# Kernel tuning notes

Measured on AMD Instinct MI355X. Metric: run time of the kernel, lower is better.

## Reference

```python
import jax, jax.numpy as jnp
import numpy as np

DIM = 512
D_STATE = 16
D_CONV = 4
EXPAND = 2
D_INNER = EXPAND * DIM  # 1024
BATCH = 4
SEQLEN = 4096


def silu(v):
    return v * jax.nn.sigmoid(v)


def setup_inputs() -> dict:
    key = jax.random.key(0)
    ks = jax.random.split(key, 8)
    s = 0.02  # small init scale for stability
    return {
        "x": jax.random.normal(ks[0], (BATCH, SEQLEN, DIM), jnp.float32),
        "W_in": jax.random.normal(ks[1], (2 * D_INNER, DIM), jnp.float32) * s,
        "conv_w": jax.random.normal(ks[2], (D_INNER, 1, D_CONV), jnp.float32) * s,
        "conv_b": jax.random.normal(ks[3], (D_INNER,), jnp.float32) * s,
        "W_x": jax.random.normal(ks[4], (2 * D_STATE, D_INNER), jnp.float32) * s,
        "W_dt": jax.random.normal(ks[5], (D_STATE, D_INNER), jnp.float32) * s,
        "b_dt": jax.random.normal(ks[6], (D_STATE,), jnp.float32) * s,
        "A_log": jnp.log(jnp.arange(1, D_STATE + 1, dtype=jnp.float32))[None, :],
        "D_param": jnp.ones((D_INNER,), jnp.float32),
        "W_out": jax.random.normal(ks[7], (DIM, D_INNER), jnp.float32) * s,
    }


def reference(x, W_in, conv_w, conv_b, W_x, W_dt, b_dt, A_log, D_param, W_out):
    B, L, _ = x.shape
    # in_proj and split into x / res streams
    x_and_res = jnp.einsum('bld,ed->ble', x, W_in)          # [B,L,2*d_inner]
    xi, res = x_and_res[..., :D_INNER], x_and_res[..., D_INNER:]
    # causal depthwise conv1d (torch pads both sides by d_conv-1 then slices [:L]
    # == left-pad d_conv-1, no right pad)
    xc = jax.lax.conv_general_dilated(
        xi.transpose(0, 2, 1), conv_w, (1,), [(D_CONV - 1, 0)],
        dimension_numbers=('NCH', 'OIH', 'NCH'), feature_group_count=D_INNER)
    xa = silu(xc.transpose(0, 2, 1) + conv_b)               # [B,L,d_inner]
    # x_proj: first d_state (dt) half is discarded in the source; keep B half
    B_proj = jnp.einsum('bld,ed->ble', xa, W_x)[..., D_STATE:]  # [B,L,N]
    dt = jax.nn.softplus(jnp.einsum('bld,nd->bln', xa, W_dt) + b_dt)  # [B,L,N]
    A = -jnp.exp(A_log.reshape(-1))                         # [N]
    A_disc = jnp.exp(A * dt)                                # [B,L,N]
    d_rep = D_INNER // D_STATE
    u = jnp.mean(xa[..., :d_rep], axis=-1)                  # [B,L] scalar drive
    Bu = (dt * B_proj) * u[..., None]                       # [B,L,N]

    def step(s, ab):
        a, b = ab
        s = s * a + b
        return s, s

    s0 = jnp.zeros((B, D_STATE), xa.dtype)
    _, y = jax.lax.scan(step, s0, (A_disc.transpose(1, 0, 2), Bu.transpose(1, 0, 2)))
    y = y.transpose(1, 0, 2)                                # [B,L,N]
    y = jnp.repeat(y, d_rep, axis=-1)                       # [B,L,d_inner]
    y = y + xa * D_param
    y = y * silu(res)
    return jnp.einsum('bld,ed->ble', y, W_out)              # [B,L,dim]
```

## Files before the change

kernel.cpp:

```cpp
#include <hip/hip_runtime.h>
#include <stdint.h>

typedef __bf16 bf16_t;
typedef __bf16 bf16x8 __attribute__((ext_vector_type(8)));
typedef __bf16 bf16x4 __attribute__((ext_vector_type(4)));
typedef float  f32x4  __attribute__((ext_vector_type(4)));

#define AS1 __attribute__((address_space(1)))
#define AS3 __attribute__((address_space(3)))

#define SEQ   4096
#define DIMM  512
#define DIN   1024
#define ROWS  16384

__device__ __forceinline__ void gload_lds16(const void* g, void* l) {
  __builtin_amdgcn_global_load_lds((AS1 void*)g, (AS3 void*)l, 16, 0, 0);
}

template<int MODE>
__global__ void gemm_bt(const bf16_t* __restrict__ A, const bf16_t* __restrict__ B,
                        void* __restrict__ Cv, int lda, int N, int K,
                        const float* __restrict__ u_g, const float* __restrict__ b_dt_g,
                        const float* __restrict__ A_log_g)
{
  __shared__ __align__(16) bf16_t As[128*64];
  __shared__ __align__(16) bf16_t Bs[128*64];
  const int tid = threadIdx.x;
  const int l = tid & 63, w = tid >> 6;
  const int bm = blockIdx.x, bn = blockIdx.y;
  const bf16_t* Ab = A + (size_t)bm*128*lda;
  const bf16_t* Bb = B + (size_t)bn*128*K;
  f32x4 acc[4][4] = {};
  const int wr = (w>>1)*64, wc = (w&1)*64;
  const int lr = l & 15, lk = (l>>4)*8;
  const int srow = w*8 + (l>>3);
  const int scol = (l&7)*8;

  for (int kt = 0; kt < K; kt += 64) {
#pragma unroll
    for (int i = 0; i < 4; i++) {
      gload_lds16(Ab + (size_t)(i*32 + srow)*lda + kt + scol, As + i*2048 + w*512);
      gload_lds16(Bb + (size_t)(i*32 + srow)*K   + kt + scol, Bs + i*2048 + w*512);
    }
    __syncthreads();
#pragma unroll
    for (int kk = 0; kk < 2; kk++) {
      bf16x8 af[4], bv[4];
#pragma unroll
      for (int m = 0; m < 4; m++) af[m] = *(const bf16x8*)&As[(wr + m*16 + lr)*64 + kk*32 + lk];
#pragma unroll
      for (int n = 0; n < 4; n++) bv[n] = *(const bf16x8*)&Bs[(wc + n*16 + lr)*64 + kk*32 + lk];
#pragma unroll
      for (int m = 0; m < 4; m++)
#pragma unroll
        for (int n = 0; n < 4; n++)
          acc[m][n] = __builtin_amdgcn_mfma_f32_16x16x32_bf16(af[m], bv[n], acc[m][n], 0, 0, 0);
    }
    __syncthreads();
  }
  const int row0 = bm*128 + wr + (l>>4)*4;
  const int col0 = bn*128 + wc + lr;

  if constexpr (MODE == 2) {
    if (wc == 0) {
      const float bdt  = b_dt_g[lr];
      const float Aexp = expf(A_log_g[lr]);
      float2* aBu = (float2*)Cv;
#pragma unroll
      for (int m = 0; m < 4; m++)
#pragma unroll
        for (int r = 0; r < 4; r++) {
          int row = row0 + m*16 + r;
          float xdt = acc[m][0][r] + bdt;
          float dt  = (xdt > 20.f) ? xdt : log1pf(expf(xdt));
          float a   = expf(-Aexp * dt);
          float Bu  = dt * acc[m][1][r] * u_g[row];
          int b = row >> 12, li = row & 4095;
          aBu[(size_t)((b<<4) + lr)*4096 + li] = make_float2(a, Bu);
        }
    }
    return;
  }

#pragma unroll
  for (int m = 0; m < 4; m++)
#pragma unroll
    for (int n = 0; n < 4; n++)
#pragma unroll
      for (int r = 0; r < 4; r++) {
        size_t idx = (size_t)(row0 + m*16 + r)*N + (col0 + n*16);
        if constexpr (MODE == 1) ((bf16_t*)Cv)[idx] = (bf16_t)acc[m][n][r];
        else                     ((float*)Cv)[idx]  = acc[m][n][r];
      }
}

__global__ __launch_bounds__(256) void convert_kernel(
    const float* __restrict__ x, const float* __restrict__ W_in,
    const float* __restrict__ W_out, const float* __restrict__ W_dt, const float* __restrict__ W_x,
    bf16_t* __restrict__ x_bf, bf16_t* __restrict__ Win_bf,
    bf16_t* __restrict__ Wout_bf, bf16_t* __restrict__ Wcat_bf)
{
  const size_t N0 = 8388608/4, N1 = N0 + 1048576/4, N2 = N1 + 524288/4, N3 = N2 + 131072/4;
  size_t i = (size_t)blockIdx.x*256 + threadIdx.x;
  bf16_t* dst; float4 v;
  if (i < N0)      { v = ((const float4*)x)[i];          dst = x_bf   + i*4; }
  else if (i < N1) { size_t j = i - N0; v = ((const float4*)W_in)[j];  dst = Win_bf  + j*4; }
  else if (i < N2) { size_t j = i - N1; v = ((const float4*)W_out)[j]; dst = Wout_bf + j*4; }
  else if (i < N3) {
    size_t j = i - N2; size_t el = j*4; int r = (int)(el >> 10), c = (int)(el & 1023);
    if (r < 16)      v = *(const float4*)(W_dt + r*1024 + c);
    else if (r < 32) v = *(const float4*)(W_x  + r*1024 + c);
    else             v = make_float4(0.f, 0.f, 0.f, 0.f);
    dst = Wcat_bf + el;
  } else return;
  bf16x4 o; o[0]=(bf16_t)v.x; o[1]=(bf16_t)v.y; o[2]=(bf16_t)v.z; o[3]=(bf16_t)v.w;
  *(bf16x4*)dst = o;
}

#define CONV_R 4
__global__ __launch_bounds__(256) void conv_kernel(
    const bf16_t* __restrict__ xi_res, const float* __restrict__ conv_w,
    const float* __restrict__ conv_b, bf16_t* __restrict__ xa, float* __restrict__ u)
{
  const int team = blockIdx.x*2 + (threadIdx.x >> 7);
  const int t    = threadIdx.x & 127;
  const int b    = team >> 10;
  const int r0   = (team & 1023) * CONV_R;
  const int c0   = t * 8;

  float w[8][4], bias[8];
#pragma unroll
  for (int e = 0; e < 8; e++) {
    float4 v = *(const float4*)(conv_w + (size_t)(c0 + e)*4);
    w[e][0]=v.x; w[e][1]=v.y; w[e][2]=v.z; w[e][3]=v.w;
  }
  {
    float4 b0 = *(const float4*)(conv_b + c0);
    float4 b1 = *(const float4*)(conv_b + c0 + 4);
    bias[0]=b0.x; bias[1]=b0.y; bias[2]=b0.z; bias[3]=b0.w;
    bias[4]=b1.x; bias[5]=b1.y; bias[6]=b1.z; bias[7]=b1.w;
  }

  const bf16_t* xbase = xi_res + ((size_t)b*SEQ + r0)*2048 + c0;
  bf16x8 rowv[CONV_R + 3];
#pragma unroll
  for (int k = 0; k < 3; k++) {
#pragma unroll
    for (int e = 0; e < 8; e++) rowv[k][e] = (bf16_t)0.f;
    if (r0 - 3 + k >= 0) rowv[k] = *(const bf16x8*)(xbase + (k - 3)*2048);
  }
#pragma unroll
  for (int k = 0; k < CONV_R; k++)
    rowv[3 + k] = *(const bf16x8*)(xbase + k*2048);

  const int growbase = b*SEQ + r0;
#pragma unroll
  for (int i = 0; i < CONV_R; i++) {
    bf16x8 o;
    float usum = 0.f;
#pragma unroll
    for (int e = 0; e < 8; e++) {
      float acc = bias[e]
        + w[e][0]*(float)rowv[i  ][e]
        + w[e][1]*(float)rowv[i+1][e]
        + w[e][2]*(float)rowv[i+2][e]
        + w[e][3]*(float)rowv[i+3][e];
      float sil = acc / (1.f + expf(-acc));
      usum += sil;
      o[e] = (bf16_t)sil;
    }
    *(bf16x8*)(xa + (size_t)(growbase + i)*DIN + c0) = o;
    if (t < 8) {
      usum += __shfl_xor(usum, 1, 64);
      usum += __shfl_xor(usum, 2, 64);
      usum += __shfl_xor(usum, 4, 64);
      if (t == 0) u[growbase + i] = usum * (1.f/64.f);
    }
  }
}

__global__ __launch_bounds__(256) void scan_kernel(const float2* __restrict__ aBu, float* __restrict__ y)
{
  __shared__ float2 lds[4096 + 256];
  __shared__ float2 wtot[4];
  const int tid = threadIdx.x;
  const int bn = blockIdx.x;
  const float2* base = aBu + (size_t)bn*4096;

#pragma unroll
  for (int c = 0; c < 16; c++) {
    int i = c*256 + tid;
    lds[i + (i>>4)] = base[i];
  }
  __syncthreads();

  const int p0 = tid*17;
  float P = 1.f, S = 0.f;
#pragma unroll
  for (int j = 0; j < 16; j++) {
    float2 ab = lds[p0 + j];
    S = S*ab.x + ab.y;
    P *= ab.x;
  }
  float Pi = P, Si = S;
  const int l = tid & 63;
#pragma unroll
  for (int off = 1; off < 64; off <<= 1) {
    float Pp = __shfl_up(Pi, off, 64);
    float Sp = __shfl_up(Si, off, 64);
    if (l >= off) { Si = Sp*Pi + Si; Pi = Pp*Pi; }
  }
  const int w = tid >> 6;
  if (l == 63) wtot[w] = make_float2(Pi, Si);
  __syncthreads();

  float Pc = 1.f, Sc = 0.f;
  for (int k = 0; k < 4; k++)
    if (k < w) { Sc = Sc*wtot[k].x + wtot[k].y; Pc *= wtot[k].x; }
  float Pe = 1.f, Se = 0.f;
  {
    float Pp = __shfl_up(Pi, 1, 64);
    float Sp = __shfl_up(Si, 1, 64);
    if (l > 0) { Pe = Pp; Se = Sp; }
  }
  float s = Sc*Pe + Se;

#pragma unroll
  for (int j = 0; j < 16; j++) {
    float2 ab = lds[p0 + j];
    s = s*ab.x + ab.y;
    lds[p0 + j].x = s;
  }
  __syncthreads();
  float* yb = y + (size_t)bn*4096;
#pragma unroll
  for (int c = 0; c < 16; c++) {
    int i = c*256 + tid;
    yb[i] = lds[i + (i>>4)].x;
  }
}

__global__ __launch_bounds__(256) void yfull_kernel(
    const bf16_t* __restrict__ xa, bf16_t* __restrict__ xi_res,
    const float* __restrict__ y_state, const float* __restrict__ D_param)
{
  int idx = blockIdx.x*256 + threadIdx.x;
  int row = idx >> 7, cc = (idx & 127)*8;
  bf16x8 xav  = *(const bf16x8*)&xa[(size_t)row*DIN + cc];
  bf16x8 resv = *(const bf16x8*)&xi_res[(size_t)row*2048 + DIN + cc];
  int b = row >> 12, li = row & 4095, n = cc >> 6;
  float ys = y_state[(size_t)((b<<4) + n)*4096 + li];
  float dp[8];
  float4 d0 = *(const float4*)(D_param + cc);
  float4 d1 = *(const float4*)(D_param + cc + 4);
  dp[0]=d0.x; dp[1]=d0.y; dp[2]=d0.z; dp[3]=d0.w; dp[4]=d1.x; dp[5]=d1.y; dp[6]=d1.z; dp[7]=d1.w;
  bf16x8 o;
#pragma unroll
  for (int e = 0; e < 8; e++) {
    float r = (float)resv[e];
    float sil = r / (1.f + expf(-r));
    float yv = (ys + (float)xav[e]*dp[e]) * sil;
    o[e] = (bf16_t)yv;
  }
  *(bf16x8*)&xi_res[(size_t)row*2048 + cc] = o;
}

extern "C" void kernel_launch(void* const* d_in, const int* in_sizes, int n_in,
                              void* d_out, int out_size, void* d_ws, size_t ws_size,
                              hipStream_t stream)
{
  const float* x      = (const float*)d_in[0];
  const float* W_in   = (const float*)d_in[1];
  const float* conv_w = (const float*)d_in[2];
  const float* conv_b = (const float*)d_in[3];
  const float* W_x    = (const float*)d_in[4];
  const float* W_dt   = (const float*)d_in[5];
  const float* b_dt   = (const float*)d_in[6];
  const float* A_log  = (const float*)d_in[7];
  const float* D_param= (const float*)d_in[8];
  const float* W_out  = (const float*)d_in[9];
  float* out = (float*)d_out;
  char* ws = (char*)d_ws;

  if (ws_size < 121700352u) return;

  const size_t MB = 1024*1024;
  bf16_t* x_bf    = (bf16_t*)(ws + 0);
  float*  y_state = (float*) (ws + 8*MB);
  bf16_t* Win_bf  = (bf16_t*)(ws + 16*MB);
  float2* aBu     = (float2*)(ws + 16*MB);
  bf16_t* Wout_bf = (bf16_t*)(ws + 18*MB);
  bf16_t* Wcat_bf = (bf16_t*)(ws + 19*MB);
  bf16_t* xi_res  = (bf16_t*)(ws + 20*MB);
  bf16_t* xa      = (bf16_t*)(ws + 84*MB);
  float*  u       = (float*) (ws + 116*MB);

  convert_kernel<<<dim3(9856), dim3(256), 0, stream>>>(x, W_in, W_out, W_dt, W_x,
                                                       x_bf, Win_bf, Wout_bf, Wcat_bf);
  gemm_bt<1><<<dim3(128,16), dim3(256), 0, stream>>>(x_bf, Win_bf, (void*)xi_res, 512, 2048, 512,
                                                     nullptr, nullptr, nullptr);
  conv_kernel<<<dim3(2048), dim3(256), 0, stream>>>(xi_res, conv_w, conv_b, xa, u);
  gemm_bt<2><<<dim3(128,1), dim3(256), 0, stream>>>(xa, Wcat_bf, (void*)aBu, 1024, 128, 1024,
                                                    u, b_dt, A_log);
  scan_kernel<<<dim3(64), dim3(256), 0, stream>>>(aBu, y_state);
  yfull_kernel<<<dim3(8192), dim3(256), 0, stream>>>(xa, xi_res, y_state, D_param);
  gemm_bt<0><<<dim3(128,4), dim3(256), 0, stream>>>(xi_res, Wout_bf, (void*)out, 2048, 512, 1024,
                                                    nullptr, nullptr, nullptr);
}
```

Before: 237.4 us.

## Replace in-projection GEMM with 256x256-tile 4-stage pipelined MFMA kernel

Adds a new gemm8 kernel for the input projection. It uses 512 threads, 256x256 output tiles, a 4-deep LDS ring of K=32 slices filled with direct global-to-LDS loads two iterations ahead, and interleaves loads between two MFMA half-phases under raised wave priority. It replaces the 128x128 gemm_bt<1> launch to raise arithmetic intensity and overlap memory with compute. The trade-offs are larger LDS use, fewer blocks (512), and reliance on hand-placed waitcnt counts for correctness. It also removes the now-unused bf16 output mode and a dead product computation in the scan.

```diff
diff --git a/kernel.cpp b/kernel.cpp
--- a/kernel.cpp
+++ b/kernel.cpp
@@ -16,6 +16,96 @@
 
 __device__ __forceinline__ void gload_lds16(const void* g, void* l) {
   __builtin_amdgcn_global_load_lds((AS1 void*)g, (AS3 void*)l, 16, 0, 0);
+}
+
+__global__ __launch_bounds__(512, 2) void gemm8(
+    const bf16_t* __restrict__ A, const bf16_t* __restrict__ B,
+    bf16_t* __restrict__ C, int lda, int ldb, int N, int K)
+{
+  __shared__ __align__(16) bf16_t Abuf[4][256*32];
+  __shared__ __align__(16) bf16_t Bbuf[4][256*32];
+  const int tid = threadIdx.x;
+  const int l = tid & 63, w = tid >> 6;
+  const int wr = w >> 2, wc = w & 3;
+  const int lr = l & 15, g = l >> 4;
+  const int bm = blockIdx.x, bn = blockIdx.y;
+  const int NT = K >> 5;
+
+  const int r0 = tid >> 2, c0e = (tid & 3) * 8;
+  const bf16_t* As0 = A + (size_t)(bm*256 +       r0)*lda + c0e;
+  const bf16_t* As1 = A + (size_t)(bm*256 + 128 + r0)*lda + c0e;
+  const bf16_t* Bs0 = B + (size_t)(bn*256 +       r0)*ldb + c0e;
+  const bf16_t* Bs1 = B + (size_t)(bn*256 + 128 + r0)*ldb + c0e;
+
+  f32x4 acc[8][4] = {};
+
+#define STAGE_A(kt_) { int d_ = (kt_) & 3; size_t ko_ = (size_t)(kt_)*32; \
+    gload_lds16(As0 + ko_, &Abuf[d_][w*512]); \
+    gload_lds16(As1 + ko_, &Abuf[d_][4096 + w*512]); }
+#define STAGE_B(kt_) { int d_ = (kt_) & 3; size_t ko_ = (size_t)(kt_)*32; \
+    gload_lds16(Bs0 + ko_, &Bbuf[d_][w*512]); \
+    gload_lds16(Bs1 + ko_, &Bbuf[d_][4096 + w*512]); }
+
+  STAGE_A(0); STAGE_B(0);
+  STAGE_A(1); STAGE_B(1);
+  asm volatile("s_waitcnt vmcnt(4)" ::: "memory");
+  __builtin_amdgcn_s_barrier();
+  __builtin_amdgcn_sched_barrier(0);
+
+  const int arow = wr*128 + lr;
+  const int brow = wc*64  + lr;
+
+  for (int kt = 0; kt < NT; ++kt) {
+    const bf16_t* Ab = Abuf[kt & 3];
+    const bf16_t* Bb = Bbuf[kt & 3];
+    bf16x8 av[4], bv[4];
+#pragma unroll
+    for (int m = 0; m < 4; m++) av[m] = *(const bf16x8*)&Ab[(arow + m*16)*32 + g*8];
+#pragma unroll
+    for (int n = 0; n < 4; n++) bv[n] = *(const bf16x8*)&Bb[(brow + n*16)*32 + g*8];
+    if (kt + 2 < NT) STAGE_A(kt + 2);
+    asm volatile("s_waitcnt lgkmcnt(0)" ::: "memory");
+    __builtin_amdgcn_sched_barrier(0);
+    __builtin_amdgcn_s_setprio(1);
+#pragma unroll
+    for (int m = 0; m < 4; m++)
+#pragma unroll
+      for (int n = 0; n < 4; n++)
+        acc[m][n] = __builtin_amdgcn_mfma_f32_16x16x32_bf16(av[m], bv[n], acc[m][n], 0, 0, 0);
+    __builtin_amdgcn_s_setprio(0);
+    __builtin_amdgcn_sched_barrier(0);
+#pragma unroll
+    for (int m = 0; m < 4; m++) av[m] = *(const bf16x8*)&Ab[(arow + 64 + m*16)*32 + g*8];
+    if (kt + 2 < NT) STAGE_B(kt + 2);
+    asm volatile("s_waitcnt lgkmcnt(0)" ::: "memory");
+    __builtin_amdgcn_sched_barrier(0);
+    __builtin_amdgcn_s_setprio(1);
+#pragma unroll
+    for (int m = 0; m < 4; m++)
+#pragma unroll
+      for (int n = 0; n < 4; n++)
+        acc[4+m][n] = __builtin_amdgcn_mfma_f32_16x16x32_bf16(av[m], bv[n], acc[4+m][n], 0, 0, 0);
+    __builtin_amdgcn_s_setprio(0);
+    __builtin_amdgcn_sched_barrier(0);
+    if (kt < NT - 1) {
+      if (kt + 2 < NT) asm volatile("s_waitcnt vmcnt(4)" ::: "memory");
+      else             asm volatile("s_waitcnt vmcnt(0)" ::: "memory");
+      __builtin_amdgcn_s_barrier();
+      __builtin_amdgcn_sched_barrier(0);
+    }
+  }
+#undef STAGE_A
+#undef STAGE_B
+
+  const int row0 = bm*256 + wr*128 + g*4;
+  const int col0 = bn*256 + wc*64 + lr;
+#pragma unroll
+  for (int m = 0; m < 8; m++)
+#pragma unroll
+    for (int n = 0; n < 4; n++)
+#pragma unroll
+      for (int r = 0; r < 4; r++)
+        C[(size_t)(row0 + m*16 + r)*N + col0 + n*16] = (bf16_t)acc[m][n][r];
 }
 
 template<int MODE>
@@ -90,8 +180,7 @@
 #pragma unroll
       for (int r = 0; r < 4; r++) {
         size_t idx = (size_t)(row0 + m*16 + r)*N + (col0 + n*16);
-        if constexpr (MODE == 1) ((bf16_t*)Cv)[idx] = (bf16_t)acc[m][n][r];
-        else                     ((float*)Cv)[idx]  = acc[m][n][r];
+        ((float*)Cv)[idx] = acc[m][n][r];
       }
 }
 
@@ -215,9 +304,9 @@
   if (l == 63) wtot[w] = make_float2(Pi, Si);
   __syncthreads();
 
-  float Pc = 1.f, Sc = 0.f;
+  float Sc = 0.f;
   for (int k = 0; k < 4; k++)
-    if (k < w) { Sc = Sc*wtot[k].x + wtot[k].y; Pc *= wtot[k].x; }
+    if (k < w) { Sc = Sc*wtot[k].x + wtot[k].y; }
   float Pe = 1.f, Se = 0.f;
   {
     float Pp = __shfl_up(Pi, 1, 64);
@@ -298,8 +387,7 @@
 
   convert_kernel<<<dim3(9856), dim3(256), 0, stream>>>(x, W_in, W_out, W_dt, W_x,
                                                        x_bf, Win_bf, Wout_bf, Wcat_bf);
-  gemm_bt<1><<<dim3(128,16), dim3(256), 0, stream>>>(x_bf, Win_bf, (void*)xi_res, 512, 2048, 512,
-                                                     nullptr, nullptr, nullptr);
+  gemm8<<<dim3(64, 8), dim3(512), 0, stream>>>(x_bf, Win_bf, xi_res, 512, 512, 2048, 512);
   conv_kernel<<<dim3(2048), dim3(256), 0, stream>>>(xi_res, conv_w, conv_b, xa, u);
   gemm_bt<2><<<dim3(128,1), dim3(256), 0, stream>>>(xa, Wcat_bf, (void*)aBu, 1024, 128, 1024,
                                                     u, b_dt, A_log);
```

After: 239.2 us. Within noise of the previous version (+0.7%).
